# Performance work log

Hardware: AMD Instinct MI355X
Metric: run time of the kernel (lower is better)

## Reference

```python
import jax, jax.numpy as jnp
import numpy as np

HID = 512
HEADS = 8
HEAD_DIM = HID // HEADS
BS, SEQ = 4, 2048


def setup_inputs() -> dict:
    key = jax.random.key(0)
    ks = jax.random.split(key, 12)
    s = 0.02
    return {
        "query": jax.random.normal(ks[0], (BS, SEQ, HID), jnp.float32),
        "key": jax.random.normal(ks[1], (BS, SEQ, HID), jnp.float32),
        "value": jax.random.normal(ks[2], (BS, SEQ, HID), jnp.float32),
        "query_mask": jnp.ones((BS, SEQ), dtype=bool),
        "key_mask": jnp.ones((BS, SEQ), dtype=bool),
        "Wq": jax.random.normal(ks[3], (HID, HID), jnp.float32) * s,
        "bq": jnp.zeros((HID,), jnp.float32),
        "Wk": jax.random.normal(ks[4], (HID, HID), jnp.float32) * s,
        "bk": jnp.zeros((HID,), jnp.float32),
        "Wv": jax.random.normal(ks[5], (HID, HID), jnp.float32) * s,
        "bv": jnp.zeros((HID,), jnp.float32),
        "Wo": jax.random.normal(ks[6], (HID, HID), jnp.float32) * s,
        "bo": jnp.zeros((HID,), jnp.float32),
    }


def _mha(query, key, value, query_mask, key_mask, Wq, bq, Wk, bk, Wv, bv, Wo, bo):
    bs, q_len, _ = query.shape
    k_len = key.shape[1]
    scale = jnp.sqrt(jnp.asarray(HEAD_DIM, query.dtype))

    def proj(x, W, b):  # nn.Linear: x @ W^T + b, then split heads -> [b,h,s,d]
        y = jnp.einsum('bse,fe->bsf', x, W) + b
        return y.reshape(bs, -1, HEADS, HEAD_DIM).transpose(0, 2, 1, 3)

    q = proj(query, Wq, bq)
    k = proj(key, Wk, bk)
    v = proj(value, Wv, bv)

    energy = jnp.einsum('bhqd,bhkd->bhqk', q, k) / scale  # [b,h,q,k]
    neg = -jnp.finfo(energy.dtype).max

    pad_mask = query_mask[:, None, :, None] & key_mask[:, None, None, :]
    energy = jnp.where(pad_mask, energy, neg)

    # causal: mask positions where q_idx < k_idx
    causal = jnp.arange(q_len)[:, None] < jnp.arange(k_len)[None, :]
    energy = jnp.where(causal[None, None], neg, energy)

    attn = jax.nn.softmax(energy, axis=-1)  # dropout p=0.0 -> identity
    x = jnp.einsum('bhqk,bhkd->bhqd', attn, v)
    x = x.transpose(0, 2, 1, 3).reshape(bs, q_len, HID)
    return jnp.einsum('bse,fe->bsf', x, Wo) + bo


def reference(query, key, value, query_mask, key_mask, Wq, bq, Wk, bk, Wv, bv, Wo, bo):
    return _mha(query, key, value, query_mask, key_mask, Wq, bq, Wk, bk, Wv, bv, Wo, bo)
```

## Files before the change

### kernel.cpp

```cpp
#include <hip/hip_runtime.h>
#include <hip/hip_bf16.h>

#define DEVI __device__ __forceinline__

typedef __attribute__((ext_vector_type(4)))  float f32x4;
typedef __attribute__((ext_vector_type(16))) float f32x16;
typedef __attribute__((ext_vector_type(8)))  short bf16x8;

constexpr int BS    = 4;
constexpr int SEQ   = 2048;
constexpr int HID   = 512;
constexpr int HEADS = 8;
constexpr int HD    = 64;
constexpr int M     = BS * SEQ;

constexpr float QSCALE = 0.125f * 1.4426950408889634f;

DEVI ushort f2bf(float f) {
    union { float f; unsigned u; } a; a.f = f;
    unsigned r = a.u + 0x7fffu + ((a.u >> 16) & 1u);
    return (ushort)(r >> 16);
}

DEVI f32x4 mfma16(bf16x8 a, bf16x8 b, f32x4 c) {
    return __builtin_amdgcn_mfma_f32_16x16x32_bf16(a, b, c, 0, 0, 0);
}
DEVI f32x16 mfma32(bf16x8 a, bf16x8 b, f32x16 c) {
    return __builtin_amdgcn_mfma_f32_32x32x16_bf16(a, b, c, 0, 0, 0);
}

DEVI void gl_lds16(const ushort* g, ushort* l) {
    __builtin_amdgcn_global_load_lds(
        (const __attribute__((address_space(1))) void*)g,
        (__attribute__((address_space(3))) void*)l,
        16, 0, 0);
}

DEVI unsigned cvtpk(float lo, float hi) {
    unsigned r;
    asm("v_cvt_pk_bf16_f32 %0, %1, %2" : "=v"(r) : "v"(lo), "v"(hi));
    return r;
}

__global__ void cast_w(const float* __restrict__ wq, const float* __restrict__ wk,
                       const float* __restrict__ wv, const float* __restrict__ wo,
                       ushort* __restrict__ oq, ushort* __restrict__ ok,
                       ushort* __restrict__ ov, ushort* __restrict__ oo)
{
    const int NW4 = HID * HID / 4;
    int i = blockIdx.x * blockDim.x + threadIdx.x;
    const int a = i >> 16, j = i & (NW4 - 1);
    const float* src = (a == 0) ? wq : (a == 1) ? wk : (a == 2) ? wv : wo;
    ushort* dst = (a == 0) ? oq : (a == 1) ? ok : (a == 2) ? ov : oo;
    float4 f = ((const float4*)src)[j];
    ushort4 u;
    u.x = f2bf(f.x); u.y = f2bf(f.y); u.z = f2bf(f.z); u.w = f2bf(f.w);
    ((ushort4*)dst)[j] = u;
}

template<bool AF32>
DEVI void gemm_core(const void* __restrict__ Ain, const ushort* __restrict__ W,
                    const float* __restrict__ bias, void* __restrict__ out,
                    float scale, int mode, ushort* lA, ushort* lB)
{
    constexpr int BK = 32, NK = HID / BK;
    const int tid  = threadIdx.x;
    const int lane = tid & 63, w = tid >> 6;
    const int wm = w >> 2, wn = w & 3;
    const int l15 = lane & 15, lg = lane >> 4;
    const int m0 = blockIdx.x * 128, n0 = blockIdx.y * 128;
    const int srow = tid >> 2, sc8 = (tid & 3) * 8;

    f32x4 acc[4][2];
    #pragma unroll
    for (int i = 0; i < 4; i++)
        #pragma unroll
        for (int n = 0; n < 2; n++) acc[i][n] = f32x4{0.f, 0.f, 0.f, 0.f};

    if constexpr (AF32) {
        const float* A = (const float*)Ain;
        const float4* ap = (const float4*)(A + (size_t)(m0 + srow) * HID + sc8);
        const float4 a0 = ap[0], a1 = ap[1];
        union { unsigned u[4]; bf16x8 v; } p;
        p.u[0] = cvtpk(a0.x, a0.y); p.u[1] = cvtpk(a0.z, a0.w);
        p.u[2] = cvtpk(a1.x, a1.y); p.u[3] = cvtpk(a1.z, a1.w);
        *(bf16x8*)(lA + srow * 32 + sc8) = p.v;
    } else {
        gl_lds16((const ushort*)Ain + (size_t)(m0 + srow) * HID + sc8, lA + w * 512);
    }
    gl_lds16(W + (size_t)(n0 + srow) * HID + sc8, lB + w * 512);
    __syncthreads();

    int cur = 0;
    for (int k = 0; k < NK; ++k) {
        ushort* lAc = lA + cur * 4096;
        ushort* lBc = lB + cur * 4096;
        ushort* lAn = lA + (cur ^ 1) * 4096;
        ushort* lBn = lB + (cur ^ 1) * 4096;
        const int k1 = (k + 1) * BK;
        const bool more = (k + 1 < NK);

        float4 a0n, a1n;
        if (more) {
            if constexpr (AF32) {
                const float* A = (const float*)Ain;
                const float4* ap = (const float4*)(A + (size_t)(m0 + srow) * HID + k1 + sc8);
                a0n = ap[0]; a1n = ap[1];
            } else {
                gl_lds16((const ushort*)Ain + (size_t)(m0 + srow) * HID + k1 + sc8,
                         lAn + w * 512);
            }
            gl_lds16(W + (size_t)(n0 + srow) * HID + k1 + sc8, lBn + w * 512);
        }

        bf16x8 af[4], bfr[2];
        #pragma unroll
        for (int i = 0; i < 4; i++)
            af[i] = *(const bf16x8*)(lAc + (wm * 64 + i * 16 + l15) * 32 + lg * 8);
        #pragma unroll
        for (int n = 0; n < 2; n++)
            bfr[n] = *(const bf16x8*)(lBc + (wn * 32 + n * 16 + l15) * 32 + lg * 8);
        #pragma unroll
        for (int i = 0; i < 4; i++)
            #pragma unroll
            for (int n = 0; n < 2; n++)
                acc[i][n] = mfma16(af[i], bfr[n], acc[i][n]);

        if (more) {
            if constexpr (AF32) {
                union { unsigned u[4]; bf16x8 v; } p;
                p.u[0] = cvtpk(a0n.x, a0n.y); p.u[1] = cvtpk(a0n.z, a0n.w);
                p.u[2] = cvtpk(a1n.x, a1n.y); p.u[3] = cvtpk(a1n.z, a1n.w);
                *(bf16x8*)(lAn + srow * 32 + sc8) = p.v;
            }
        }
        __syncthreads();
        cur ^= 1;
    }

    #pragma unroll
    for (int i = 0; i < 4; i++) {
        #pragma unroll
        for (int n = 0; n < 2; n++) {
            const int col = n0 + wn * 32 + n * 16 + l15;
            const float bb = bias[col];
            const int rbase = m0 + wm * 64 + i * 16 + lg * 4;
            #pragma unroll
            for (int jj = 0; jj < 4; jj++) {
                float v = (acc[i][n][jj] + bb) * scale;
                const int r = rbase + jj;
                if (mode == 3) {
                    ((float*)out)[(size_t)r * HID + col] = v;
                } else {
                    const int b = r >> 11, s = r & (SEQ - 1);
                    const int h = col >> 6, d = col & 63;
                    const int bh = b * HEADS + h;
                    const int t = s >> 5;
                    const ushort u = f2bf(v);
                    if (mode == 0) {
                        const int l31r = s & 31;
                        const int ds = d >> 4, hif = (d >> 3) & 1, jf = d & 7;
                        ((ushort*)out)[(((size_t)bh * 64 + t) * 4 + ds) * 512 +
                                       (hif * 32 + l31r) * 8 + jf] = u;
                    } else {
                        const int c = s & 31;
                        const int kvh = (c >> 4) & 1, hif = (c >> 2) & 1;
                        const int jf = (c & 3) + ((c >> 3) & 1) * 4;
                        const int dt = d >> 5, drow = d & 31;
                        ((ushort*)out)[(((size_t)bh * 64 + t) * 4 + dt * 2 + kvh) * 512 +
                                       (hif * 32 + drow) * 8 + jf] = u;
                    }
                }
            }
        }
    }
}

__global__ __launch_bounds__(512, 4)
void gemm_qkv(const float* __restrict__ Xq, const float* __restrict__ Xk,
              const float* __restrict__ Xv,
              const ushort* __restrict__ Wq, const ushort* __restrict__ Wk,
              const ushort* __restrict__ Wv,
              const float* __restrict__ bq, const float* __restrict__ bk,
              const float* __restrict__ bv,
              ushort* __restrict__ Qf, ushort* __restrict__ Kf,
              ushort* __restrict__ Vf)
{
    __shared__ ushort lA[2 * 128 * 32];
    __shared__ ushort lB[2 * 128 * 32];
    const int z = blockIdx.z;
    const float* A = z == 0 ? Xq : z == 1 ? Xk : Xv;
    const ushort* W = z == 0 ? Wq : z == 1 ? Wk : Wv;
    const float* bias = z == 0 ? bq : z == 1 ? bk : bv;
    void* out = z == 0 ? (void*)Qf : z == 1 ? (void*)Kf : (void*)Vf;
    gemm_core<true>(A, W, bias, out, z == 0 ? QSCALE : 1.0f, z == 2 ? 2 : 0, lA, lB);
}

__global__ __launch_bounds__(512, 4)
void gemm_o(const ushort* __restrict__ ctx, const ushort* __restrict__ Wo,
            const float* __restrict__ bo, float* __restrict__ out)
{
    __shared__ ushort lA[2 * 128 * 32];
    __shared__ ushort lB[2 * 128 * 32];
    gemm_core<false>(ctx, Wo, bo, out, 1.0f, 3, lA, lB);
}

__global__ __launch_bounds__(256)
void attn5(const ushort* __restrict__ Qf, const ushort* __restrict__ Kf,
           const ushort* __restrict__ Vf, ushort* __restrict__ ctx)
{
    __shared__ float part[4][2][16][64];
    __shared__ float pml[4][2][32];

    const int tid  = threadIdx.x;
    const int lane = tid & 63, w = tid >> 6;
    const int l31 = lane & 31, hi = lane >> 5;

    const int bid = blockIdx.x;
    const int bh  = bid & 31;
    const int qt  = 63 - (bid >> 5);
    const int qb  = qt * 32;

    const ushort* Qb = Qf + ((size_t)bh * 64 + qt) * 2048;
    const ushort* Kb = Kf + (size_t)bh * 64 * 2048;
    const ushort* Vb = Vf + (size_t)bh * 64 * 2048;

    bf16x8 qf[4];
    #pragma unroll
    for (int ds = 0; ds < 4; ds++)
        qf[ds] = *(const bf16x8*)(Qb + ds * 512 + lane * 8);

    f32x16 acc0 = {}, acc1 = {};
    float mrun = -3e38f, lrun = 0.f;

    bf16x8 kf[4] = {}, va[4] = {};
    if (w <= qt) {
        const ushort* kp = Kb + (size_t)w * 2048 + lane * 8;
        const ushort* vp = Vb + (size_t)w * 2048 + lane * 8;
        #pragma unroll
        for (int ds = 0; ds < 4; ds++) {
            kf[ds] = *(const bf16x8*)(kp + ds * 512);
            va[ds] = *(const bf16x8*)(vp + ds * 512);
        }
    }

    for (int t = w; t <= qt; t += 4) {
        f32x16 s = {};
        #pragma unroll
        for (int ds = 0; ds < 4; ds++)
            s = mfma32(kf[ds], qf[ds], s);

        bf16x8 kfn[4], van[4];
        {
            const int tn = (t + 4 <= qt) ? t + 4 : t;
            const ushort* kp = Kb + (size_t)tn * 2048 + lane * 8;
            const ushort* vp = Vb + (size_t)tn * 2048 + lane * 8;
            #pragma unroll
            for (int ds = 0; ds < 4; ds++) {
                kfn[ds] = *(const bf16x8*)(kp + ds * 512);
                van[ds] = *(const bf16x8*)(vp + ds * 512);
            }
        }

        if (t == qt) {
            #pragma unroll
            for (int r = 0; r < 16; r++) {
                const int kvrow = (r & 3) + 8 * (r >> 2) + 4 * hi;
                s[r] = (kvrow > l31) ? -3e38f : s[r];
            }
        }

        float m8[8];
        #pragma unroll
        for (int r = 0; r < 8; r++) m8[r] = fmaxf(s[r], s[r + 8]);
        float m4a = fmaxf(m8[0], m8[1]), m4b = fmaxf(m8[2], m8[3]);
        float m4c = fmaxf(m8[4], m8[5]), m4d = fmaxf(m8[6], m8[7]);
        float pmax = fmaxf(fmaxf(m4a, m4b), fmaxf(m4c, m4d));
        pmax = fmaxf(pmax, __shfl_xor(pmax, 32));

        if (!__all(pmax <= mrun + 8.f)) {
            const float mnew = fmaxf(mrun, pmax);
            const float corr = __builtin_amdgcn_exp2f(mrun - mnew);
            lrun *= corr;
            #pragma unroll
            for (int r = 0; r < 16; r++) { acc0[r] *= corr; acc1[r] *= corr; }
            mrun = mnew;
        }

        float e[16];
        #pragma unroll
        for (int r = 0; r < 16; r++)
            e[r] = __builtin_amdgcn_exp2f(s[r] - mrun);
        float es0 = (e[0] + e[1]) + (e[2] + e[3]);
        float es1 = (e[4] + e[5]) + (e[6] + e[7]);
        float es2 = (e[8] + e[9]) + (e[10] + e[11]);
        float es3 = (e[12] + e[13]) + (e[14] + e[15]);
        float esum = (es0 + es1) + (es2 + es3);
        lrun += esum + __shfl_xor(esum, 32);

        union { unsigned u[4]; bf16x8 v; } pb0, pb1;
        pb0.u[0] = cvtpk(e[0],  e[1]);  pb0.u[1] = cvtpk(e[2],  e[3]);
        pb0.u[2] = cvtpk(e[4],  e[5]);  pb0.u[3] = cvtpk(e[6],  e[7]);
        pb1.u[0] = cvtpk(e[8],  e[9]);  pb1.u[1] = cvtpk(e[10], e[11]);
        pb1.u[2] = cvtpk(e[12], e[13]); pb1.u[3] = cvtpk(e[14], e[15]);

        acc0 = mfma32(va[0], pb0.v, acc0);
        acc0 = mfma32(va[1], pb1.v, acc0);
        acc1 = mfma32(va[2], pb0.v, acc1);
        acc1 = mfma32(va[3], pb1.v, acc1);

        #pragma unroll
        for (int ds = 0; ds < 4; ds++) { kf[ds] = kfn[ds]; va[ds] = van[ds]; }
    }

    #pragma unroll
    for (int r = 0; r < 16; r++) {
        part[w][0][r][lane] = acc0[r];
        part[w][1][r][lane] = acc1[r];
    }
    if (hi == 0) { pml[w][0][l31] = mrun; pml[w][1][l31] = lrun; }
    __syncthreads();

    const float mm0 = pml[0][0][l31], ll0 = pml[0][1][l31];
    const float mm1 = pml[1][0][l31], ll1 = pml[1][1][l31];
    const float mm2 = pml[2][0][l31], ll2 = pml[2][1][l31];
    const float mm3 = pml[3][0][l31], ll3 = pml[3][1][l31];
    const float mstar = fmaxf(fmaxf(mm0, mm1), fmaxf(mm2, mm3));
    const float f0 = __builtin_amdgcn_exp2f(mm0 - mstar);
    const float f1 = __builtin_amdgcn_exp2f(mm1 - mstar);
    const float f2 = __builtin_amdgcn_exp2f(mm2 - mstar);
    const float f3 = __builtin_amdgcn_exp2f(mm3 - mstar);
    const float lstar = ll0 * f0 + ll1 * f1 + ll2 * f2 + ll3 * f3;
    const float inv = 1.f / lstar;

    const int b = bh >> 3, h = bh & 7;
    ushort* op = ctx + ((size_t)(b * SEQ + qb + l31)) * HID + h * HD;
    #pragma unroll
    for (int a = 0; a < 2; a++) {
        float v[4];
        #pragma unroll
        for (int j = 0; j < 4; j++) {
            const int r = 4 * w + j;
            v[j] = (part[0][a][r][lane] * f0 + part[1][a][r][lane] * f1 +
                    part[2][a][r][lane] * f2 + part[3][a][r][lane] * f3) * inv;
        }
        ushort4 o;
        o.x = f2bf(v[0]); o.y = f2bf(v[1]); o.z = f2bf(v[2]); o.w = f2bf(v[3]);
        *(ushort4*)(op + a * 32 + 8 * w + 4 * hi) = o;
    }
}

extern "C" void kernel_launch(void* const* d_in, const int* in_sizes, int n_in,
                              void* d_out, int out_size, void* d_ws, size_t ws_size,
                              hipStream_t stream) {
    const float* q  = (const float*)d_in[0];
    const float* k  = (const float*)d_in[1];
    const float* v  = (const float*)d_in[2];
    const float* Wq = (const float*)d_in[5];
    const float* bq = (const float*)d_in[6];
    const float* Wk = (const float*)d_in[7];
    const float* bk = (const float*)d_in[8];
    const float* Wv = (const float*)d_in[9];
    const float* bv = (const float*)d_in[10];
    const float* Wo = (const float*)d_in[11];
    const float* bo = (const float*)d_in[12];

    char* ws = (char*)d_ws;
    constexpr size_t XSZ = (size_t)M * HID * 2;
    constexpr size_t WSZ = (size_t)HID * HID * 2;
    ushort* Wqb = (ushort*)(ws);
    ushort* Wkb = (ushort*)(ws + WSZ);
    ushort* Wvb = (ushort*)(ws + 2 * WSZ);
    ushort* Wob = (ushort*)(ws + 3 * WSZ);
    ushort* Qf  = (ushort*)(ws + 4 * WSZ);
    ushort* Kf  = (ushort*)(ws + 4 * WSZ + XSZ);
    ushort* Vf  = (ushort*)(ws + 4 * WSZ + 2 * XSZ);
    ushort* ctx = (ushort*)(ws + 4 * WSZ + 3 * XSZ);

    cast_w<<<1024, 256, 0, stream>>>(Wq, Wk, Wv, Wo, Wqb, Wkb, Wvb, Wob);

    dim3 gqkv(M / 128, HID / 128, 3);
    gemm_qkv<<<gqkv, 512, 0, stream>>>(q, k, v, Wqb, Wkb, Wvb,
                                       bq, bk, bv, Qf, Kf, Vf);

    attn5<<<BS * HEADS * (SEQ / 32), 256, 0, stream>>>(Qf, Kf, Vf, ctx);

    dim3 go(M / 128, HID / 128);
    gemm_o<<<go, 512, 0, stream>>>(ctx, Wob, bo, (float*)d_out);
}
```

Measured before the change: 91.62 us.

## Pre-cast activations to bf16 and use direct-to-LDS loads with fragment-ordered layout

```diff
diff --git a/kernel.cpp b/kernel.cpp
--- a/kernel.cpp
+++ b/kernel.cpp
@@ -40,6 +40,24 @@
     unsigned r;
     asm("v_cvt_pk_bf16_f32 %0, %1, %2" : "=v"(r) : "v"(lo), "v"(hi));
     return r;
+}
+
+__global__ void cast_x(const float* __restrict__ q, const float* __restrict__ k,
+                       const float* __restrict__ v,
+                       ushort* __restrict__ oq, ushort* __restrict__ ok,
+                       ushort* __restrict__ ov)
+{
+    const size_t NQ4 = (size_t)M * HID / 4;
+    for (size_t i = (size_t)blockIdx.x * blockDim.x + threadIdx.x; i < 3 * NQ4;
+         i += (size_t)gridDim.x * blockDim.x) {
+        const size_t a = i / NQ4, j = i - a * NQ4;
+        const float* src = (a == 0) ? q : (a == 1) ? k : v;
+        ushort* dst = (a == 0) ? oq : (a == 1) ? ok : ov;
+        float4 f = ((const float4*)src)[j];
+        ushort4 u;
+        u.x = f2bf(f.x); u.y = f2bf(f.y); u.z = f2bf(f.z); u.w = f2bf(f.w);
+        ((ushort4*)dst)[j] = u;
+    }
 }
 
 __global__ void cast_w(const float* __restrict__ wq, const float* __restrict__ wk,
@@ -58,8 +76,7 @@
     ((ushort4*)dst)[j] = u;
 }
 
-template<bool AF32>
-DEVI void gemm_core(const void* __restrict__ Ain, const ushort* __restrict__ W,
+DEVI void gemm_core(const ushort* __restrict__ A, const ushort* __restrict__ W,
                     const float* __restrict__ bias, void* __restrict__ out,
                     float scale, int mode, ushort* lA, ushort* lB)
 {
@@ -69,7 +86,11 @@
     const int wm = w >> 2, wn = w & 3;
     const int l15 = lane & 15, lg = lane >> 4;
     const int m0 = blockIdx.x * 128, n0 = blockIdx.y * 128;
-    const int srow = tid >> 2, sc8 = (tid & 3) * 8;
+    const int fr = lane & 15;
+    const int fc = (lane >> 4) * 8;
+
+    const ushort* Arow = A + (size_t)(m0 + 16 * w + fr) * HID + fc;
+    const ushort* Wrow = W + (size_t)(n0 + 16 * w + fr) * HID + fc;
 
     f32x4 acc[4][2];
     #pragma unroll
@@ -77,18 +98,8 @@
         #pragma unroll
         for (int n = 0; n < 2; n++) acc[i][n] = f32x4{0.f, 0.f, 0.f, 0.f};
 
-    if constexpr (AF32) {
-        const float* A = (const float*)Ain;
-        const float4* ap = (const float4*)(A + (size_t)(m0 + srow) * HID + sc8);
-        const float4 a0 = ap[0], a1 = ap[1];
-        union { unsigned u[4]; bf16x8 v; } p;
-        p.u[0] = cvtpk(a0.x, a0.y); p.u[1] = cvtpk(a0.z, a0.w);
-        p.u[2] = cvtpk(a1.x, a1.y); p.u[3] = cvtpk(a1.z, a1.w);
-        *(bf16x8*)(lA + srow * 32 + sc8) = p.v;
-    } else {
-        gl_lds16((const ushort*)Ain + (size_t)(m0 + srow) * HID + sc8, lA + w * 512);
-    }
-    gl_lds16(W + (size_t)(n0 + srow) * HID + sc8, lB + w * 512);
+    gl_lds16(Arow, lA + w * 512);
+    gl_lds16(Wrow, lB + w * 512);
     __syncthreads();
 
     int cur = 0;
@@ -97,43 +108,25 @@
         ushort* lBc = lB + cur * 4096;
         ushort* lAn = lA + (cur ^ 1) * 4096;
         ushort* lBn = lB + (cur ^ 1) * 4096;
-        const int k1 = (k + 1) * BK;
-        const bool more = (k + 1 < NK);
-
-        float4 a0n, a1n;
-        if (more) {
-            if constexpr (AF32) {
-                const float* A = (const float*)Ain;
-                const float4* ap = (const float4*)(A + (size_t)(m0 + srow) * HID + k1 + sc8);
-                a0n = ap[0]; a1n = ap[1];
-            } else {
-                gl_lds16((const ushort*)Ain + (size_t)(m0 + srow) * HID + k1 + sc8,
-                         lAn + w * 512);
-            }
-            gl_lds16(W + (size_t)(n0 + srow) * HID + k1 + sc8, lBn + w * 512);
+
+        if (k + 1 < NK) {
+            gl_lds16(Arow + (k + 1) * BK, lAn + w * 512);
+            gl_lds16(Wrow + (k + 1) * BK, lBn + w * 512);
         }
 
         bf16x8 af[4], bfr[2];
         #pragma unroll
         for (int i = 0; i < 4; i++)
-            af[i] = *(const bf16x8*)(lAc + (wm * 64 + i * 16 + l15) * 32 + lg * 8);
+            af[i] = *(const bf16x8*)(lAc + (wm * 4 + i) * 512 + lane * 8);
         #pragma unroll
         for (int n = 0; n < 2; n++)
-            bfr[n] = *(const bf16x8*)(lBc + (wn * 32 + n * 16 + l15) * 32 + lg * 8);
+            bfr[n] = *(const bf16x8*)(lBc + (wn * 2 + n) * 512 + lane * 8);
         #pragma unroll
         for (int i = 0; i < 4; i++)
             #pragma unroll
             for (int n = 0; n < 2; n++)
                 acc[i][n] = mfma16(af[i], bfr[n], acc[i][n]);
 
-        if (more) {
-            if constexpr (AF32) {
-                union { unsigned u[4]; bf16x8 v; } p;
-                p.u[0] = cvtpk(a0n.x, a0n.y); p.u[1] = cvtpk(a0n.z, a0n.w);
-                p.u[2] = cvtpk(a1n.x, a1n.y); p.u[3] = cvtpk(a1n.z, a1n.w);
-                *(bf16x8*)(lAn + srow * 32 + sc8) = p.v;
-            }
-        }
         __syncthreads();
         cur ^= 1;
     }
@@ -177,8 +170,8 @@
 }
 
 __global__ __launch_bounds__(512, 4)
-void gemm_qkv(const float* __restrict__ Xq, const float* __restrict__ Xk,
-              const float* __restrict__ Xv,
+void gemm_qkv(const ushort* __restrict__ Xq, const ushort* __restrict__ Xk,
+              const ushort* __restrict__ Xv,
               const ushort* __restrict__ Wq, const ushort* __restrict__ Wk,
               const ushort* __restrict__ Wv,
               const float* __restrict__ bq, const float* __restrict__ bk,
@@ -186,23 +179,23 @@
               ushort* __restrict__ Qf, ushort* __restrict__ Kf,
               ushort* __restrict__ Vf)
 {
-    __shared__ ushort lA[2 * 128 * 32];
-    __shared__ ushort lB[2 * 128 * 32];
+    __shared__ ushort lA[2 * 8 * 512];
+    __shared__ ushort lB[2 * 8 * 512];
     const int z = blockIdx.z;
-    const float* A = z == 0 ? Xq : z == 1 ? Xk : Xv;
+    const ushort* A = z == 0 ? Xq : z == 1 ? Xk : Xv;
     const ushort* W = z == 0 ? Wq : z == 1 ? Wk : Wv;
     const float* bias = z == 0 ? bq : z == 1 ? bk : bv;
     void* out = z == 0 ? (void*)Qf : z == 1 ? (void*)Kf : (void*)Vf;
-    gemm_core<true>(A, W, bias, out, z == 0 ? QSCALE : 1.0f, z == 2 ? 2 : 0, lA, lB);
+    gemm_core(A, W, bias, out, z == 0 ? QSCALE : 1.0f, z == 2 ? 2 : 0, lA, lB);
 }
 
 __global__ __launch_bounds__(512, 4)
 void gemm_o(const ushort* __restrict__ ctx, const ushort* __restrict__ Wo,
             const float* __restrict__ bo, float* __restrict__ out)
 {
-    __shared__ ushort lA[2 * 128 * 32];
-    __shared__ ushort lB[2 * 128 * 32];
-    gemm_core<false>(ctx, Wo, bo, out, 1.0f, 3, lA, lB);
+    __shared__ ushort lA[2 * 8 * 512];
+    __shared__ ushort lB[2 * 8 * 512];
+    gemm_core(ctx, Wo, bo, out, 1.0f, 3, lA, lB);
 }
 
 __global__ __launch_bounds__(256)
@@ -372,15 +365,19 @@
     ushort* Wkb = (ushort*)(ws + WSZ);
     ushort* Wvb = (ushort*)(ws + 2 * WSZ);
     ushort* Wob = (ushort*)(ws + 3 * WSZ);
-    ushort* Qf  = (ushort*)(ws + 4 * WSZ);
-    ushort* Kf  = (ushort*)(ws + 4 * WSZ + XSZ);
-    ushort* Vf  = (ushort*)(ws + 4 * WSZ + 2 * XSZ);
-    ushort* ctx = (ushort*)(ws + 4 * WSZ + 3 * XSZ);
+    ushort* Xq  = (ushort*)(ws + 4 * WSZ);
+    ushort* Xk  = (ushort*)(ws + 4 * WSZ + XSZ);
+    ushort* Xv  = (ushort*)(ws + 4 * WSZ + 2 * XSZ);
+    ushort* Qf  = (ushort*)(ws + 4 * WSZ + 3 * XSZ);
+    ushort* Kf  = (ushort*)(ws + 4 * WSZ + 4 * XSZ);
+    ushort* Vf  = (ushort*)(ws + 4 * WSZ + 5 * XSZ);
+    ushort* ctx = (ushort*)(ws + 4 * WSZ + 6 * XSZ);
 
     cast_w<<<1024, 256, 0, stream>>>(Wq, Wk, Wv, Wo, Wqb, Wkb, Wvb, Wob);
+    cast_x<<<2048, 256, 0, stream>>>(q, k, v, Xq, Xk, Xv);
 
     dim3 gqkv(M / 128, HID / 128, 3);
-    gemm_qkv<<<gqkv, 512, 0, stream>>>(q, k, v, Wqb, Wkb, Wvb,
+    gemm_qkv<<<gqkv, 512, 0, stream>>>(Xq, Xk, Xv, Wqb, Wkb, Wvb,
                                        bq, bk, bv, Qf, Kf, Vf);
 
     attn5<<<BS * HEADS * (SEQ / 32), 256, 0, stream>>>(Qf, Kf, Vf, ctx);
```

After: 106.6 us. 16.4% more time.
